# Optimization experiments

Hardware: AMD Instinct MI355X
Metric: run time of the kernel (lower is better)

Reference implementation:

```python
import jax, jax.numpy as jnp
import numpy as np

N, E, F_IN, DIM, HEADS = 16384, 262144, 128, 64, 4
HID = DIM * HEADS  # 256
NEG = 0.2


def _lin(k, fan_in, fan_out):
    kw, kb = jax.random.split(k)
    s = 1.0 / np.sqrt(fan_in)
    return (jax.random.uniform(kw, (fan_in, fan_out), jnp.float32, -s, s),
            jax.random.uniform(kb, (fan_out,), jnp.float32, -s, s))


def setup_inputs() -> dict:
    key = jax.random.key(0)
    ks = jax.random.split(key, 20)
    x = jax.random.normal(ks[0], (N, F_IN), jnp.float32)
    edge_index = jax.random.randint(ks[1], (2, E), 0, N, jnp.int32)
    Win, b_in = _lin(ks[2], F_IN, DIM)
    Wskip, bskip = _lin(ks[3], DIM, HID)
    # conv1: in=DIM, out per head=DIM, heads=HEADS, concat -> HID
    Wl1, _ = _lin(ks[4], DIM, HID)
    Wr1, _ = _lin(ks[5], DIM, HID)
    att1 = jax.random.normal(ks[6], (HEADS, DIM), jnp.float32) * 0.1
    b1 = jnp.zeros((HID,), jnp.float32)
    # conv2: in=HID, out=HID, heads=1, concat=False
    Wl2, _ = _lin(ks[7], HID, HID)
    Wr2, _ = _lin(ks[8], HID, HID)
    att2 = jax.random.normal(ks[9], (1, HID), jnp.float32) * 0.1
    b2 = jnp.zeros((HID,), jnp.float32)
    # conv3: in=HID, out=HID, heads=1, concat=False
    Wl3, _ = _lin(ks[10], HID, HID)
    Wr3, _ = _lin(ks[11], HID, HID)
    att3 = jax.random.normal(ks[12], (1, HID), jnp.float32) * 0.1
    b3 = jnp.zeros((HID,), jnp.float32)
    Wm1, bm1 = _lin(ks[13], HID, DIM)
    Wm2, bm2 = _lin(ks[14], DIM, DIM)
    Wm3, bm3 = _lin(ks[15], DIM, 1)
    return dict(x=x, edge_index=edge_index, Win=Win, b_in=b_in,
                Wskip=Wskip, bskip=bskip,
                Wl1=Wl1, Wr1=Wr1, att1=att1, b1=b1,
                Wl2=Wl2, Wr2=Wr2, att2=att2, b2=b2,
                Wl3=Wl3, Wr3=Wr3, att3=att3, b3=b3,
                Wm1=Wm1, bm1=bm1, Wm2=Wm2, bm2=bm2, Wm3=Wm3, bm3=bm3)


def gatv2(x, src, dst, Wl, Wr, att, b, concat):
    # PyG GATv2Conv: x_l = lin_l(x)[src], x_r = lin_r(x)[dst]
    n = x.shape[0]
    H, D = att.shape
    xl = (x @ Wl).reshape(n, H, D)
    xr = (x @ Wr).reshape(n, H, D)
    e = jax.nn.leaky_relu(xl[src] + xr[dst], NEG)          # [E, H, D]
    logits = jnp.einsum('ehd,hd->eh', e, att)              # [E, H]
    m = jax.ops.segment_max(logits, dst, num_segments=n)   # per-dst softmax
    alpha = jnp.exp(logits - m[dst])
    denom = jax.ops.segment_sum(alpha, dst, num_segments=n)
    alpha = alpha / denom[dst]
    out = jax.ops.segment_sum(alpha[:, :, None] * xl[src], dst, num_segments=n)
    out = out.reshape(n, H * D) if concat else out.mean(axis=1)
    return out + b


def reference(x, edge_index, Win, b_in, Wskip, bskip,
              Wl1, Wr1, att1, b1, Wl2, Wr2, att2, b2,
              Wl3, Wr3, att3, b3, Wm1, bm1, Wm2, bm2, Wm3, bm3):
    n = x.shape[0]
    # add self loops (GATv2Conv default add_self_loops=True)
    loop = jnp.arange(n, dtype=edge_index.dtype)
    src = jnp.concatenate([edge_index[0], loop])
    dst = jnp.concatenate([edge_index[1], loop])

    h = jax.nn.relu(x @ Win + b_in)                         # [N, DIM]
    out1 = jax.nn.relu(gatv2(h, src, dst, Wl1, Wr1, att1, b1, True))
    out1 = out1 + (h @ Wskip + bskip)                       # [N, HID]
    out2 = jax.nn.relu(gatv2(out1, src, dst, Wl2, Wr2, att2, b2, False))
    out2 = out2 + out1
    out3 = jax.nn.relu(gatv2(out2, src, dst, Wl3, Wr3, att3, b3, False))
    out3 = out3 + out2
    out = jax.nn.relu(out3 @ Wm1 + bm1)
    out = jax.nn.relu(out @ Wm2 + bm2)
    out = out @ Wm3 + bm3                                   # [N, 1]
    return out.reshape(-1)
```

## Files before the change

kernel.cpp:

```cpp
#include <hip/hip_runtime.h>
#include <cstdint>
#include <cstddef>

#define N_NODES 16384
#define E_EDGES 262144
#define FIN     128
#define DIM     64
#define HID     256
#define NEG     0.2f

typedef _Float16 h8 __attribute__((ext_vector_type(8)));
typedef _Float16 h4 __attribute__((ext_vector_type(4)));
typedef float    f32x4 __attribute__((ext_vector_type(4)));

__global__ __launch_bounds__(256) void zero_cnt_kernel(int4* __restrict__ cnt) {
    cnt[blockIdx.x * 256 + threadIdx.x] = make_int4(0, 0, 0, 0);
}

__global__ __launch_bounds__(256) void hist_kernel(const int* __restrict__ dst,
                                                   int* __restrict__ cnt) {
    int i = blockIdx.x * 256 + threadIdx.x;
    if (i < E_EDGES) atomicAdd(&cnt[dst[i]], 1);
}

__global__ __launch_bounds__(256) void csr_scan_kernel(const int* __restrict__ cnt,
                                                       int* __restrict__ offs,
                                                       int* __restrict__ cursor) {
    __shared__ int bs[256];
    __shared__ int psum[257];
    int tid = threadIdx.x;
    int base = tid * 64;
    int s = 0;
    for (int i = 0; i < 64; ++i) s += cnt[base + i];
    bs[tid] = s;
    __syncthreads();
    if (tid == 0) {
        int r = 0;
        for (int i = 0; i < 256; ++i) { psum[i] = r; r += bs[i]; }
        psum[256] = r;
    }
    __syncthreads();
    int run = psum[tid];
    for (int i = 0; i < 64; ++i) {
        int c = cnt[base + i];
        offs[base + i] = run;
        cursor[base + i] = run;
        run += c;
    }
    if (tid == 255) offs[N_NODES] = run;
}

__global__ __launch_bounds__(256) void scatter_kernel(const int* __restrict__ src,
                                                      const int* __restrict__ dst,
                                                      int* __restrict__ cursor,
                                                      int* __restrict__ esrc) {
    int i = blockIdx.x * 256 + threadIdx.x;
    if (i < E_EDGES) {
        int p = atomicAdd(&cursor[dst[i]], 1);
        esrc[p] = src[i];
    }
}

struct PackJob { const float* W; _Float16* dst; int Ksrc, Nsrc, NT, colOff; };
struct PackJobs { PackJob j[10]; };

__global__ __launch_bounds__(256) void pack_all_kernel(PackJobs jobs) {
    PackJob jb = jobs.j[blockIdx.y];
    int i = blockIdx.x * 256 + threadIdx.x;
    if (i < jb.Ksrc * jb.Nsrc) {
        int k = i / jb.Nsrc, n = i % jb.Nsrc;
        jb.dst[((size_t)(k >> 3) * jb.NT + jb.colOff + n) * 8 + (k & 7)] = (_Float16)jb.W[i];
    }
}

template<int K, bool RELU, bool O16, bool IN32>
__global__ __launch_bounds__(64) void mfma_n64_kernel(const void* __restrict__ Av,
                                                      const _Float16* __restrict__ Wp,
                                                      const float* __restrict__ bias,
                                                      void* __restrict__ outv) {
    int lane = threadIdx.x;
    int rowBase = blockIdx.x * 64;
    int l15 = lane & 15, l4 = lane >> 4;

    f32x4 acc[4][4] = {};
#pragma unroll
    for (int ks = 0; ks < K / 32; ++ks) {
        h8 af[4], bf[4];
#pragma unroll
        for (int mi = 0; mi < 4; ++mi) {
            if constexpr (IN32) {
                const float* ap = (const float*)Av + (size_t)(rowBase + mi * 16 + l15) * K + ks * 32 + l4 * 8;
                float4 a0 = *(const float4*)ap;
                float4 a1 = *(const float4*)(ap + 4);
                h8 v;
                v[0] = (_Float16)a0.x; v[1] = (_Float16)a0.y;
                v[2] = (_Float16)a0.z; v[3] = (_Float16)a0.w;
                v[4] = (_Float16)a1.x; v[5] = (_Float16)a1.y;
                v[6] = (_Float16)a1.z; v[7] = (_Float16)a1.w;
                af[mi] = v;
            } else {
                af[mi] = *(const h8*)((const _Float16*)Av + (size_t)(rowBase + mi * 16 + l15) * K + ks * 32 + l4 * 8);
            }
        }
#pragma unroll
        for (int ni = 0; ni < 4; ++ni)
            bf[ni] = *(const h8*)(Wp + ((size_t)(ks * 4 + l4) * 64 + ni * 16 + l15) * 8);
#pragma unroll
        for (int mi = 0; mi < 4; ++mi)
#pragma unroll
            for (int ni = 0; ni < 4; ++ni)
                acc[mi][ni] = __builtin_amdgcn_mfma_f32_16x16x32_f16(af[mi], bf[ni], acc[mi][ni], 0, 0, 0);
    }
#pragma unroll
    for (int mi = 0; mi < 4; ++mi)
#pragma unroll
        for (int ni = 0; ni < 4; ++ni) {
            int c = ni * 16 + l15;
            float bv = bias[c];
#pragma unroll
            for (int q = 0; q < 4; ++q) {
                int r = rowBase + mi * 16 + l4 * 4 + q;
                float v = acc[mi][ni][q] + bv;
                if (RELU) v = fmaxf(v, 0.f);
                if constexpr (O16) ((_Float16*)outv)[(size_t)r * 64 + c] = (_Float16)v;
                else               ((float*)outv)[(size_t)r * 64 + c] = v;
            }
        }
}

template<int K>
__global__ __launch_bounds__(256) void mfma_gemm_kernel(const _Float16* __restrict__ A,
                                                        const _Float16* __restrict__ Wp,
                                                        int NT,
                                                        _Float16* __restrict__ o16a,
                                                        _Float16* __restrict__ o16b,
                                                        float* __restrict__ o32,
                                                        const float* __restrict__ bias) {
    int tid = threadIdx.x;
    int lane = tid & 63, wid = tid >> 6;
    int wm = wid >> 1, wn = wid & 1;
    int rowBase = blockIdx.x * 128 + wm * 64;
    int colBase = blockIdx.y * 128 + wn * 64;
    int l15 = lane & 15, l4 = lane >> 4;

    f32x4 acc[4][4] = {};
#pragma unroll
    for (int ks = 0; ks < K / 32; ++ks) {
        h8 af[4], bf[4];
#pragma unroll
        for (int mi = 0; mi < 4; ++mi)
            af[mi] = *(const h8*)(A + (size_t)(rowBase + mi * 16 + l15) * K + ks * 32 + l4 * 8);
#pragma unroll
        for (int ni = 0; ni < 4; ++ni)
            bf[ni] = *(const h8*)(Wp + ((size_t)(ks * 4 + l4) * NT + colBase + ni * 16 + l15) * 8);
#pragma unroll
        for (int mi = 0; mi < 4; ++mi)
#pragma unroll
            for (int ni = 0; ni < 4; ++ni)
                acc[mi][ni] = __builtin_amdgcn_mfma_f32_16x16x32_f16(af[mi], bf[ni], acc[mi][ni], 0, 0, 0);
    }

    int seg = colBase >> 8;
    int cbase = colBase & 255;
    if (o32 != nullptr && seg == 2) {
#pragma unroll
        for (int mi = 0; mi < 4; ++mi)
#pragma unroll
            for (int ni = 0; ni < 4; ++ni) {
                int c = cbase + ni * 16 + l15;
                float bv = bias[c];
#pragma unroll
                for (int q = 0; q < 4; ++q) {
                    int r = rowBase + mi * 16 + l4 * 4 + q;
                    o32[(size_t)r * 256 + c] = acc[mi][ni][q] + bv;
                }
            }
    } else {
        _Float16* o = (seg == 0) ? o16a : o16b;
#pragma unroll
        for (int mi = 0; mi < 4; ++mi)
#pragma unroll
            for (int ni = 0; ni < 4; ++ni) {
                int c = cbase + ni * 16 + l15;
#pragma unroll
                for (int q = 0; q < 4; ++q) {
                    int r = rowBase + mi * 16 + l4 * 4 + q;
                    o[(size_t)r * 256 + c] = (_Float16)acc[mi][ni][q];
                }
            }
    }
}

template<int H, int OMODE>
__global__ __launch_bounds__(256) void gat_agg_kernel(const _Float16* __restrict__ xl,
                                                      const _Float16* __restrict__ xr,
                                                      const float* __restrict__ att,
                                                      const float* __restrict__ bias,
                                                      const float* __restrict__ resid,
                                                      const int* __restrict__ offs,
                                                      const int* __restrict__ esrc,
                                                      float* __restrict__ out,
                                                      _Float16* __restrict__ out16) {
    int wid = threadIdx.x >> 6;
    int lane = threadIdx.x & 63;
    int node = blockIdx.x * 4 + wid;

    auto ld4 = [&](const _Float16* p, int n) -> float4 {
        h4 v = *(const h4*)(p + ((size_t)n << 8) + (lane << 2));
        return make_float4((float)v[0], (float)v[1], (float)v[2], (float)v[3]);
    };

    float4 xrv = ld4(xr, node);
    float4 av = ((const float4*)att)[lane];

    float m = -1e30f, s = 0.f;
    float4 acc = make_float4(0.f, 0.f, 0.f, 0.f);

    auto logit = [&](const float4& xlv) -> float {
        float ex = xlv.x + xrv.x; ex = ex > 0.f ? ex : NEG * ex;
        float ey = xlv.y + xrv.y; ey = ey > 0.f ? ey : NEG * ey;
        float ez = xlv.z + xrv.z; ez = ez > 0.f ? ez : NEG * ez;
        float ew = xlv.w + xrv.w; ew = ew > 0.f ? ew : NEG * ew;
        float lp = ex * av.x + ey * av.y + ez * av.z + ew * av.w;
        lp += __shfl_xor(lp, 1);
        lp += __shfl_xor(lp, 2);
        lp += __shfl_xor(lp, 4);
        lp += __shfl_xor(lp, 8);
        if constexpr (H == 1) {
            lp += __shfl_xor(lp, 16);
            lp += __shfl_xor(lp, 32);
        }
        return lp;
    };

    auto single = [&](int src) {
        float4 xlv = ld4(xl, src);
        float lp = logit(xlv);
        float mn = fmaxf(m, lp);
        float c = __expf(m - mn);
        float p = __expf(lp - mn);
        s = s * c + p;
        acc.x = acc.x * c + p * xlv.x;
        acc.y = acc.y * c + p * xlv.y;
        acc.z = acc.z * c + p * xlv.z;
        acc.w = acc.w * c + p * xlv.w;
        m = mn;
    };

    single(node);
    int e0 = offs[node], e1 = offs[node + 1];
    int e = e0;
    for (; e + 8 <= e1; e += 8) {
        float4 xv[8]; float lp[8], pp[8];
#pragma unroll
        for (int j = 0; j < 8; ++j) xv[j] = ld4(xl, esrc[e + j]);
#pragma unroll
        for (int j = 0; j < 8; ++j) lp[j] = logit(xv[j]);
        float mn = m;
#pragma unroll
        for (int j = 0; j < 8; ++j) mn = fmaxf(mn, lp[j]);
        float c = __expf(m - mn);
#pragma unroll
        for (int j = 0; j < 8; ++j) pp[j] = __expf(lp[j] - mn);
        float ps = 0.f;
        float4 pa = make_float4(0.f, 0.f, 0.f, 0.f);
#pragma unroll
        for (int j = 0; j < 8; ++j) {
            ps += pp[j];
            pa.x += pp[j] * xv[j].x;
            pa.y += pp[j] * xv[j].y;
            pa.z += pp[j] * xv[j].z;
            pa.w += pp[j] * xv[j].w;
        }
        s = s * c + ps;
        acc.x = acc.x * c + pa.x;
        acc.y = acc.y * c + pa.y;
        acc.z = acc.z * c + pa.z;
        acc.w = acc.w * c + pa.w;
        m = mn;
    }
    for (; e + 4 <= e1; e += 4) {
        float4 xv[4]; float lp[4], pp[4];
#pragma unroll
        for (int j = 0; j < 4; ++j) xv[j] = ld4(xl, esrc[e + j]);
#pragma unroll
        for (int j = 0; j < 4; ++j) lp[j] = logit(xv[j]);
        float mn = fmaxf(fmaxf(fmaxf(lp[0], lp[1]), fmaxf(lp[2], lp[3])), m);
        float c = __expf(m - mn);
#pragma unroll
        for (int j = 0; j < 4; ++j) pp[j] = __expf(lp[j] - mn);
        s = s * c + ((pp[0] + pp[1]) + (pp[2] + pp[3]));
        acc.x = acc.x * c + ((pp[0] * xv[0].x + pp[1] * xv[1].x) + (pp[2] * xv[2].x + pp[3] * xv[3].x));
        acc.y = acc.y * c + ((pp[0] * xv[0].y + pp[1] * xv[1].y) + (pp[2] * xv[2].y + pp[3] * xv[3].y));
        acc.z = acc.z * c + ((pp[0] * xv[0].z + pp[1] * xv[1].z) + (pp[2] * xv[2].z + pp[3] * xv[3].z));
        acc.w = acc.w * c + ((pp[0] * xv[0].w + pp[1] * xv[1].w) + (pp[2] * xv[2].w + pp[3] * xv[3].w));
        m = mn;
    }
    for (; e < e1; ++e) single(esrc[e]);

    float inv = 1.f / s;
    float4 bv = ((const float4*)bias)[lane];
    float4 rv = ((const float4*)resid)[((size_t)node << 6) + lane];
    float4 o;
    o.x = fmaxf(acc.x * inv + bv.x, 0.f) + rv.x;
    o.y = fmaxf(acc.y * inv + bv.y, 0.f) + rv.y;
    o.z = fmaxf(acc.z * inv + bv.z, 0.f) + rv.z;
    o.w = fmaxf(acc.w * inv + bv.w, 0.f) + rv.w;
    if constexpr (OMODE != 2)
        ((float4*)out)[((size_t)node << 6) + lane] = o;
    if constexpr (OMODE != 0) {
        h4 ov;
        ov[0] = (_Float16)o.x; ov[1] = (_Float16)o.y;
        ov[2] = (_Float16)o.z; ov[3] = (_Float16)o.w;
        *(h4*)(out16 + ((size_t)node << 8) + (lane << 2)) = ov;
    }
}

__global__ __launch_bounds__(64) void mlp_head_kernel(const _Float16* __restrict__ A,
                                                      const _Float16* __restrict__ Wm1p,
                                                      const float* __restrict__ bm1,
                                                      const _Float16* __restrict__ Wm2p,
                                                      const float* __restrict__ bm2,
                                                      const float* __restrict__ Wm3,
                                                      const float* __restrict__ bm3,
                                                      float* __restrict__ out) {
    __shared__ _Float16 t1s[64][72];
    int lane = threadIdx.x;
    int rowBase = blockIdx.x * 64;
    int l15 = lane & 15, l4 = lane >> 4;

    f32x4 acc[4][4] = {};
#pragma unroll
    for (int ks = 0; ks < 8; ++ks) {
        h8 af[4], bf[4];
#pragma unroll
        for (int mi = 0; mi < 4; ++mi)
            af[mi] = *(const h8*)(A + (size_t)(rowBase + mi * 16 + l15) * 256 + ks * 32 + l4 * 8);
#pragma unroll
        for (int ni = 0; ni < 4; ++ni)
            bf[ni] = *(const h8*)(Wm1p + ((size_t)(ks * 4 + l4) * 64 + ni * 16 + l15) * 8);
#pragma unroll
        for (int mi = 0; mi < 4; ++mi)
#pragma unroll
            for (int ni = 0; ni < 4; ++ni)
                acc[mi][ni] = __builtin_amdgcn_mfma_f32_16x16x32_f16(af[mi], bf[ni], acc[mi][ni], 0, 0, 0);
    }
#pragma unroll
    for (int mi = 0; mi < 4; ++mi)
#pragma unroll
        for (int ni = 0; ni < 4; ++ni) {
            int c = ni * 16 + l15;
            float bv = bm1[c];
#pragma unroll
            for (int q = 0; q < 4; ++q)
                t1s[mi * 16 + l4 * 4 + q][c] = (_Float16)fmaxf(acc[mi][ni][q] + bv, 0.f);
        }

    f32x4 acc2[4][4] = {};
#pragma unroll
    for (int ks = 0; ks < 2; ++ks) {
        h8 af[4], bf[4];
#pragma unroll
        for (int mi = 0; mi < 4; ++mi)
            af[mi] = *(const h8*)&t1s[mi * 16 + l15][ks * 32 + l4 * 8];
#pragma unroll
        for (int ni = 0; ni < 4; ++ni)
            bf[ni] = *(const h8*)(Wm2p + ((size_t)(ks * 4 + l4) * 64 + ni * 16 + l15) * 8);
#pragma unroll
        for (int mi = 0; mi < 4; ++mi)
#pragma unroll
            for (int ni = 0; ni < 4; ++ni)
                acc2[mi][ni] = __builtin_amdgcn_mfma_f32_16x16x32_f16(af[mi], bf[ni], acc2[mi][ni], 0, 0, 0);
    }

    float b3 = bm3[0];
    float b2v[4], w3v[4];
#pragma unroll
    for (int ni = 0; ni < 4; ++ni) {
        b2v[ni] = bm2[ni * 16 + l15];
        w3v[ni] = Wm3[ni * 16 + l15];
    }
#pragma unroll
    for (int mi = 0; mi < 4; ++mi)
#pragma unroll
        for (int q = 0; q < 4; ++q) {
            float part = 0.f;
#pragma unroll
            for (int ni = 0; ni < 4; ++ni)
                part += fmaxf(acc2[mi][ni][q] + b2v[ni], 0.f) * w3v[ni];
            part += __shfl_xor(part, 1);
            part += __shfl_xor(part, 2);
            part += __shfl_xor(part, 4);
            part += __shfl_xor(part, 8);
            if (l15 == 0)
                out[rowBase + mi * 16 + l4 * 4 + q] = part + b3;
        }
}

extern "C" void kernel_launch(void* const* d_in, const int* in_sizes, int n_in,
                              void* d_out, int out_size, void* d_ws, size_t ws_size,
                              hipStream_t stream) {
    const float* x     = (const float*)d_in[0];
    const int*   ei    = (const int*)d_in[1];
    const float* Win   = (const float*)d_in[2];
    const float* b_in  = (const float*)d_in[3];
    const float* Wskip = (const float*)d_in[4];
    const float* bskip = (const float*)d_in[5];
    const float* Wl1   = (const float*)d_in[6];
    const float* Wr1   = (const float*)d_in[7];
    const float* att1  = (const float*)d_in[8];
    const float* b1    = (const float*)d_in[9];
    const float* Wl2   = (const float*)d_in[10];
    const float* Wr2   = (const float*)d_in[11];
    const float* att2  = (const float*)d_in[12];
    const float* b2    = (const float*)d_in[13];
    const float* Wl3   = (const float*)d_in[14];
    const float* Wr3   = (const float*)d_in[15];
    const float* att3  = (const float*)d_in[16];
    const float* b3    = (const float*)d_in[17];
    const float* Wm1   = (const float*)d_in[18];
    const float* bm1   = (const float*)d_in[19];
    const float* Wm2   = (const float*)d_in[20];
    const float* bm2   = (const float*)d_in[21];
    const float* Wm3   = (const float*)d_in[22];
    const float* bm3   = (const float*)d_in[23];

    char* p = (char*)d_ws;
    auto alloc = [&](size_t bytes) { char* r = p; p += (bytes + 255) & ~(size_t)255; return r; };
    const size_t NN = N_NODES;
    float*    skip = (float*)alloc(NN * 256 * 4);
    float*    out1 = (float*)alloc(NN * 256 * 4);
    _Float16* o116 = (_Float16*)alloc(NN * 256 * 2);
    _Float16* o216 = (_Float16*)alloc(NN * 256 * 2);
    _Float16* o316 = o116;
    _Float16* h16  = (_Float16*)alloc(NN * 64 * 2);
    _Float16* xl16 = (_Float16*)alloc(NN * 256 * 2);
    _Float16* xr16 = (_Float16*)alloc(NN * 256 * 2);
    _Float16* Wp1  = (_Float16*)alloc((size_t)64 * 768 * 2);
    _Float16* Wp2  = (_Float16*)alloc((size_t)256 * 512 * 2);
    _Float16* Wp3  = (_Float16*)alloc((size_t)256 * 512 * 2);
    _Float16* Winp = (_Float16*)alloc((size_t)128 * 64 * 2);
    _Float16* Wm1p = (_Float16*)alloc((size_t)256 * 64 * 2);
    _Float16* Wm2p = (_Float16*)alloc((size_t)64 * 64 * 2);
    int* cnt    = (int*)alloc(N_NODES * 4);
    int* offs   = (int*)alloc((N_NODES + 1) * 4);
    int* cursor = (int*)alloc(N_NODES * 4);
    int* esrc   = (int*)alloc(E_EDGES * 4);

    const int* src = ei;
    const int* dst = ei + E_EDGES;

    zero_cnt_kernel<<<N_NODES / 1024, 256, 0, stream>>>((int4*)cnt);
    hist_kernel<<<E_EDGES / 256, 256, 0, stream>>>(dst, cnt);
    csr_scan_kernel<<<1, 256, 0, stream>>>(cnt, offs, cursor);
    scatter_kernel<<<E_EDGES / 256, 256, 0, stream>>>(src, dst, cursor, esrc);

    PackJobs jobs = {{
        { Wl1,   Wp1,  64,  256, 768, 0   },
        { Wr1,   Wp1,  64,  256, 768, 256 },
        { Wskip, Wp1,  64,  256, 768, 512 },
        { Wl2,   Wp2,  256, 256, 512, 0   },
        { Wr2,   Wp2,  256, 256, 512, 256 },
        { Wl3,   Wp3,  256, 256, 512, 0   },
        { Wr3,   Wp3,  256, 256, 512, 256 },
        { Win,   Winp, 128, 64,  64,  0   },
        { Wm1,   Wm1p, 256, 64,  64,  0   },
        { Wm2,   Wm2p, 64,  64,  64,  0   },
    }};
    pack_all_kernel<<<dim3(256, 10), 256, 0, stream>>>(jobs);

    mfma_n64_kernel<128, true, true, true><<<N_NODES / 64, 64, 0, stream>>>(x, Winp, b_in, h16);

    mfma_gemm_kernel<64><<<dim3(128, 6), 256, 0, stream>>>(h16, Wp1, 768, xl16, xr16, skip, bskip);
    gat_agg_kernel<4, 1><<<N_NODES / 4, 256, 0, stream>>>(xl16, xr16, att1, b1, skip, offs, esrc, out1, o116);

    mfma_gemm_kernel<256><<<dim3(128, 4), 256, 0, stream>>>(o116, Wp2, 512, xl16, xr16, nullptr, nullptr);
    gat_agg_kernel<1, 1><<<N_NODES / 4, 256, 0, stream>>>(xl16, xr16, att2, b2, out1, offs, esrc, skip , o216);

    mfma_gemm_kernel<256><<<dim3(128, 4), 256, 0, stream>>>(o216, Wp3, 512, xl16, xr16, nullptr, nullptr);
    gat_agg_kernel<1, 2><<<N_NODES / 4, 256, 0, stream>>>(xl16, xr16, att3, b3, skip , offs, esrc, nullptr, o316);

    mlp_head_kernel<<<N_NODES / 64, 64, 0, stream>>>(o316, Wm1p, bm1, Wm2p, bm2, Wm3, bm3, (float*)d_out);
}
```

Baseline: 225.5 us.

## Split each node's edge aggregation across four waves with LDS softmax merge

The GAT aggregation kernel now assigns one block per destination node instead of one wave per node. The four waves take interleaved edges, keep their own online-softmax state, and merge it through shared memory using max rescaling. The goal is more parallelism per node and better load balance across uneven degrees, at the cost of a block barrier, LDS traffic, and three waves sitting idle during the final merge. The grid grows to N blocks.

```diff
diff --git a/kernel.cpp b/kernel.cpp
--- a/kernel.cpp
+++ b/kernel.cpp
@@ -201,9 +201,13 @@
                                                       const int* __restrict__ esrc,
                                                       float* __restrict__ out,
                                                       _Float16* __restrict__ out16) {
+    __shared__ float  lm[3][64];
+    __shared__ float  lssum[3][64];
+    __shared__ float4 lacc[3][64];
+
     int wid = threadIdx.x >> 6;
     int lane = threadIdx.x & 63;
-    int node = blockIdx.x * 4 + wid;
+    int node = blockIdx.x;
 
     auto ld4 = [&](const _Float16* p, int n) -> float4 {
         h4 v = *(const h4*)(p + ((size_t)n << 8) + (lane << 2));
@@ -247,42 +251,13 @@
         m = mn;
     };
 
-    single(node);
+    if (wid == 0) single(node);
     int e0 = offs[node], e1 = offs[node + 1];
-    int e = e0;
-    for (; e + 8 <= e1; e += 8) {
-        float4 xv[8]; float lp[8], pp[8];
-#pragma unroll
-        for (int j = 0; j < 8; ++j) xv[j] = ld4(xl, esrc[e + j]);
-#pragma unroll
-        for (int j = 0; j < 8; ++j) lp[j] = logit(xv[j]);
-        float mn = m;
-#pragma unroll
-        for (int j = 0; j < 8; ++j) mn = fmaxf(mn, lp[j]);
-        float c = __expf(m - mn);
-#pragma unroll
-        for (int j = 0; j < 8; ++j) pp[j] = __expf(lp[j] - mn);
-        float ps = 0.f;
-        float4 pa = make_float4(0.f, 0.f, 0.f, 0.f);
-#pragma unroll
-        for (int j = 0; j < 8; ++j) {
-            ps += pp[j];
-            pa.x += pp[j] * xv[j].x;
-            pa.y += pp[j] * xv[j].y;
-            pa.z += pp[j] * xv[j].z;
-            pa.w += pp[j] * xv[j].w;
-        }
-        s = s * c + ps;
-        acc.x = acc.x * c + pa.x;
-        acc.y = acc.y * c + pa.y;
-        acc.z = acc.z * c + pa.z;
-        acc.w = acc.w * c + pa.w;
-        m = mn;
-    }
-    for (; e + 4 <= e1; e += 4) {
+    int e = e0 + wid;
+    for (; e + 12 < e1; e += 16) {
         float4 xv[4]; float lp[4], pp[4];
 #pragma unroll
-        for (int j = 0; j < 4; ++j) xv[j] = ld4(xl, esrc[e + j]);
+        for (int j = 0; j < 4; ++j) xv[j] = ld4(xl, esrc[e + 4 * j]);
 #pragma unroll
         for (int j = 0; j < 4; ++j) lp[j] = logit(xv[j]);
         float mn = fmaxf(fmaxf(fmaxf(lp[0], lp[1]), fmaxf(lp[2], lp[3])), m);
@@ -296,16 +271,41 @@
         acc.w = acc.w * c + ((pp[0] * xv[0].w + pp[1] * xv[1].w) + (pp[2] * xv[2].w + pp[3] * xv[3].w));
         m = mn;
     }
-    for (; e < e1; ++e) single(esrc[e]);
-
-    float inv = 1.f / s;
+    for (; e < e1; e += 4) single(esrc[e]);
+
+    if (wid != 0) {
+        lm[wid - 1][lane] = m;
+        lssum[wid - 1][lane] = s;
+        lacc[wid - 1][lane] = acc;
+    }
+    __syncthreads();
+    if (wid != 0) return;
+
+    float M = m;
+#pragma unroll
+    for (int w = 0; w < 3; ++w) M = fmaxf(M, lm[w][lane]);
+    float c0 = __expf(m - M);
+    float stot = s * c0;
+    float4 atot = make_float4(acc.x * c0, acc.y * c0, acc.z * c0, acc.w * c0);
+#pragma unroll
+    for (int w = 0; w < 3; ++w) {
+        float cw = __expf(lm[w][lane] - M);
+        float4 aw = lacc[w][lane];
+        stot += lssum[w][lane] * cw;
+        atot.x += aw.x * cw;
+        atot.y += aw.y * cw;
+        atot.z += aw.z * cw;
+        atot.w += aw.w * cw;
+    }
+
+    float inv = 1.f / stot;
     float4 bv = ((const float4*)bias)[lane];
     float4 rv = ((const float4*)resid)[((size_t)node << 6) + lane];
     float4 o;
-    o.x = fmaxf(acc.x * inv + bv.x, 0.f) + rv.x;
-    o.y = fmaxf(acc.y * inv + bv.y, 0.f) + rv.y;
-    o.z = fmaxf(acc.z * inv + bv.z, 0.f) + rv.z;
-    o.w = fmaxf(acc.w * inv + bv.w, 0.f) + rv.w;
+    o.x = fmaxf(atot.x * inv + bv.x, 0.f) + rv.x;
+    o.y = fmaxf(atot.y * inv + bv.y, 0.f) + rv.y;
+    o.z = fmaxf(atot.z * inv + bv.z, 0.f) + rv.z;
+    o.w = fmaxf(atot.w * inv + bv.w, 0.f) + rv.w;
     if constexpr (OMODE != 2)
         ((float4*)out)[((size_t)node << 6) + lane] = o;
     if constexpr (OMODE != 0) {
@@ -472,13 +472,13 @@
     mfma_n64_kernel<128, true, true, true><<<N_NODES / 64, 64, 0, stream>>>(x, Winp, b_in, h16);
 
     mfma_gemm_kernel<64><<<dim3(128, 6), 256, 0, stream>>>(h16, Wp1, 768, xl16, xr16, skip, bskip);
-    gat_agg_kernel<4, 1><<<N_NODES / 4, 256, 0, stream>>>(xl16, xr16, att1, b1, skip, offs, esrc, out1, o116);
+    gat_agg_kernel<4, 1><<<N_NODES, 256, 0, stream>>>(xl16, xr16, att1, b1, skip, offs, esrc, out1, o116);
 
     mfma_gemm_kernel<256><<<dim3(128, 4), 256, 0, stream>>>(o116, Wp2, 512, xl16, xr16, nullptr, nullptr);
-    gat_agg_kernel<1, 1><<<N_NODES / 4, 256, 0, stream>>>(xl16, xr16, att2, b2, out1, offs, esrc, skip , o216);
+    gat_agg_kernel<1, 1><<<N_NODES, 256, 0, stream>>>(xl16, xr16, att2, b2, out1, offs, esrc, skip , o216);
 
     mfma_gemm_kernel<256><<<dim3(128, 4), 256, 0, stream>>>(o216, Wp3, 512, xl16, xr16, nullptr, nullptr);
-    gat_agg_kernel<1, 2><<<N_NODES / 4, 256, 0, stream>>>(xl16, xr16, att3, b3, skip , offs, esrc, nullptr, o316);
+    gat_agg_kernel<1, 2><<<N_NODES, 256, 0, stream>>>(xl16, xr16, att3, b3, skip , offs, esrc, nullptr, o316);
 
     mlp_head_kernel<<<N_NODES / 64, 64, 0, stream>>>(o316, Wm1p, bm1, Wm2p, bm2, Wm3, bm3, (float*)d_out);
 }
```

Measured after the change: 235.7 us. 1.05x slower.

## Split GAT aggregation wave into four edge groups with packed fp16 logits

Applied to the files above, without the earlier changes.

The GAT aggregation kernel now splits each wave into four 16-lane groups. Each group processes a different incoming edge, and each lane covers 16 feature dims loaded as two 16-byte vectors. The logit is computed in packed fp16 (add, leaky-relu via max, fdot2) with fewer shuffle steps per edge. Per-group online-softmax states are merged by an xor butterfly before the output is written. This cuts the serial per-edge dependency chain and the reduction cost, but drops the 8-edge batched ILP, adds a 16-value cross-group merge, and computes logits at reduced fp16 precision.

```diff
diff --git a/kernel.cpp b/kernel.cpp
--- a/kernel.cpp
+++ b/kernel.cpp
@@ -11,6 +11,7 @@
 
 typedef _Float16 h8 __attribute__((ext_vector_type(8)));
 typedef _Float16 h4 __attribute__((ext_vector_type(4)));
+typedef _Float16 h2 __attribute__((ext_vector_type(2)));
 typedef float    f32x4 __attribute__((ext_vector_type(4)));
 
 __global__ __launch_bounds__(256) void zero_cnt_kernel(int4* __restrict__ cnt) {
@@ -201,118 +202,110 @@
                                                       const int* __restrict__ esrc,
                                                       float* __restrict__ out,
                                                       _Float16* __restrict__ out16) {
-    int wid = threadIdx.x >> 6;
-    int lane = threadIdx.x & 63;
+    int tid = threadIdx.x;
+    int wid = tid >> 6;
+    int lane = tid & 63;
     int node = blockIdx.x * 4 + wid;
-
-    auto ld4 = [&](const _Float16* p, int n) -> float4 {
-        h4 v = *(const h4*)(p + ((size_t)n << 8) + (lane << 2));
-        return make_float4((float)v[0], (float)v[1], (float)v[2], (float)v[3]);
-    };
-
-    float4 xrv = ld4(xr, node);
-    float4 av = ((const float4*)att)[lane];
+    int g  = lane >> 4;
+    int li = lane & 15;
+
+    h2 xrv[8];
+    {
+        const h8* xp = (const h8*)(xr + ((size_t)node << 8) + (li << 4));
+        h8 a0 = xp[0], a1 = xp[1];
+#pragma unroll
+        for (int i = 0; i < 4; ++i) { xrv[i][0] = a0[2 * i]; xrv[i][1] = a0[2 * i + 1]; }
+#pragma unroll
+        for (int i = 0; i < 4; ++i) { xrv[4 + i][0] = a1[2 * i]; xrv[4 + i][1] = a1[2 * i + 1]; }
+    }
+    h2 attv[8];
+    {
+        const float4* ap = (const float4*)(att + (li << 4));
+#pragma unroll
+        for (int i = 0; i < 4; ++i) {
+            float4 a = ap[i];
+            attv[2 * i][0] = (_Float16)a.x; attv[2 * i][1] = (_Float16)a.y;
+            attv[2 * i + 1][0] = (_Float16)a.z; attv[2 * i + 1][1] = (_Float16)a.w;
+        }
+    }
+    const h2 negc = { (_Float16)NEG, (_Float16)NEG };
 
     float m = -1e30f, s = 0.f;
-    float4 acc = make_float4(0.f, 0.f, 0.f, 0.f);
-
-    auto logit = [&](const float4& xlv) -> float {
-        float ex = xlv.x + xrv.x; ex = ex > 0.f ? ex : NEG * ex;
-        float ey = xlv.y + xrv.y; ey = ey > 0.f ? ey : NEG * ey;
-        float ez = xlv.z + xrv.z; ez = ez > 0.f ? ez : NEG * ez;
-        float ew = xlv.w + xrv.w; ew = ew > 0.f ? ew : NEG * ew;
-        float lp = ex * av.x + ey * av.y + ez * av.z + ew * av.w;
-        lp += __shfl_xor(lp, 1);
-        lp += __shfl_xor(lp, 2);
-        lp += __shfl_xor(lp, 4);
-        lp += __shfl_xor(lp, 8);
+    float acc[16];
+#pragma unroll
+    for (int i = 0; i < 16; ++i) acc[i] = 0.f;
+
+    int e0 = offs[node];
+    int total = offs[node + 1] - e0 + 1;
+
+    for (int vi = g; vi < total; vi += 4) {
+        int srcn = (vi == 0) ? node : esrc[e0 + vi - 1];
+        const h8* xp = (const h8*)(xl + ((size_t)srcn << 8) + (li << 4));
+        h8 a0 = xp[0], a1 = xp[1];
+
+        float part = 0.f;
+        float xf[16];
+#pragma unroll
+        for (int i = 0; i < 8; ++i) {
+            h2 v;
+            if (i < 4) { v[0] = a0[2 * i]; v[1] = a0[2 * i + 1]; }
+            else       { v[0] = a1[2 * (i - 4)]; v[1] = a1[2 * (i - 4) + 1]; }
+            xf[2 * i]     = (float)v[0];
+            xf[2 * i + 1] = (float)v[1];
+            h2 sum = v + xrv[i];
+            h2 lr = __builtin_elementwise_max(sum, sum * negc);
+            part = __builtin_amdgcn_fdot2(lr, attv[i], part, false);
+        }
+        part += __shfl_xor(part, 1);
+        part += __shfl_xor(part, 2);
         if constexpr (H == 1) {
-            lp += __shfl_xor(lp, 16);
-            lp += __shfl_xor(lp, 32);
-        }
-        return lp;
-    };
-
-    auto single = [&](int src) {
-        float4 xlv = ld4(xl, src);
-        float lp = logit(xlv);
+            part += __shfl_xor(part, 4);
+            part += __shfl_xor(part, 8);
+        }
+        float lp = part;
+
         float mn = fmaxf(m, lp);
         float c = __expf(m - mn);
         float p = __expf(lp - mn);
         s = s * c + p;
-        acc.x = acc.x * c + p * xlv.x;
-        acc.y = acc.y * c + p * xlv.y;
-        acc.z = acc.z * c + p * xlv.z;
-        acc.w = acc.w * c + p * xlv.w;
+#pragma unroll
+        for (int i = 0; i < 16; ++i) acc[i] = acc[i] * c + p * xf[i];
         m = mn;
-    };
-
-    single(node);
-    int e0 = offs[node], e1 = offs[node + 1];
-    int e = e0;
-    for (; e + 8 <= e1; e += 8) {
-        float4 xv[8]; float lp[8], pp[8];
-#pragma unroll
-        for (int j = 0; j < 8; ++j) xv[j] = ld4(xl, esrc[e + j]);
-#pragma unroll
-        for (int j = 0; j < 8; ++j) lp[j] = logit(xv[j]);
-        float mn = m;
-#pragma unroll
-        for (int j = 0; j < 8; ++j) mn = fmaxf(mn, lp[j]);
-        float c = __expf(m - mn);
-#pragma unroll
-        for (int j = 0; j < 8; ++j) pp[j] = __expf(lp[j] - mn);
-        float ps = 0.f;
-        float4 pa = make_float4(0.f, 0.f, 0.f, 0.f);
-#pragma unroll
-        for (int j = 0; j < 8; ++j) {
-            ps += pp[j];
-            pa.x += pp[j] * xv[j].x;
-            pa.y += pp[j] * xv[j].y;
-            pa.z += pp[j] * xv[j].z;
-            pa.w += pp[j] * xv[j].w;
-        }
-        s = s * c + ps;
-        acc.x = acc.x * c + pa.x;
-        acc.y = acc.y * c + pa.y;
-        acc.z = acc.z * c + pa.z;
-        acc.w = acc.w * c + pa.w;
-        m = mn;
-    }
-    for (; e + 4 <= e1; e += 4) {
-        float4 xv[4]; float lp[4], pp[4];
-#pragma unroll
-        for (int j = 0; j < 4; ++j) xv[j] = ld4(xl, esrc[e + j]);
-#pragma unroll
-        for (int j = 0; j < 4; ++j) lp[j] = logit(xv[j]);
-        float mn = fmaxf(fmaxf(fmaxf(lp[0], lp[1]), fmaxf(lp[2], lp[3])), m);
-        float c = __expf(m - mn);
-#pragma unroll
-        for (int j = 0; j < 4; ++j) pp[j] = __expf(lp[j] - mn);
-        s = s * c + ((pp[0] + pp[1]) + (pp[2] + pp[3]));
-        acc.x = acc.x * c + ((pp[0] * xv[0].x + pp[1] * xv[1].x) + (pp[2] * xv[2].x + pp[3] * xv[3].x));
-        acc.y = acc.y * c + ((pp[0] * xv[0].y + pp[1] * xv[1].y) + (pp[2] * xv[2].y + pp[3] * xv[3].y));
-        acc.z = acc.z * c + ((pp[0] * xv[0].z + pp[1] * xv[1].z) + (pp[2] * xv[2].z + pp[3] * xv[3].z));
-        acc.w = acc.w * c + ((pp[0] * xv[0].w + pp[1] * xv[1].w) + (pp[2] * xv[2].w + pp[3] * xv[3].w));
-        m = mn;
-    }
-    for (; e < e1; ++e) single(esrc[e]);
+    }
+
+#pragma unroll
+    for (int mask = 16; mask <= 32; mask <<= 1) {
+        float m2 = __shfl_xor(m, mask);
+        float s2 = __shfl_xor(s, mask);
+        float M = fmaxf(m, m2);
+        float c1 = __expf(m - M);
+        float c2 = __expf(m2 - M);
+        s = s * c1 + s2 * c2;
+#pragma unroll
+        for (int i = 0; i < 16; ++i) {
+            float a2 = __shfl_xor(acc[i], mask);
+            acc[i] = acc[i] * c1 + a2 * c2;
+        }
+        m = M;
+    }
 
     float inv = 1.f / s;
-    float4 bv = ((const float4*)bias)[lane];
-    float4 rv = ((const float4*)resid)[((size_t)node << 6) + lane];
-    float4 o;
-    o.x = fmaxf(acc.x * inv + bv.x, 0.f) + rv.x;
-    o.y = fmaxf(acc.y * inv + bv.y, 0.f) + rv.y;
-    o.z = fmaxf(acc.z * inv + bv.z, 0.f) + rv.z;
-    o.w = fmaxf(acc.w * inv + bv.w, 0.f) + rv.w;
-    if constexpr (OMODE != 2)
-        ((float4*)out)[((size_t)node << 6) + lane] = o;
+    int dbase = (li << 4) + (g << 2);
+    float4 bv = *(const float4*)(bias + dbase);
+    float4 rv = *(const float4*)(resid + ((size_t)node << 8) + dbase);
+    float o0 = fmaxf(acc[(g << 2) + 0] * inv + bv.x, 0.f) + rv.x;
+    float o1 = fmaxf(acc[(g << 2) + 1] * inv + bv.y, 0.f) + rv.y;
+    float o2 = fmaxf(acc[(g << 2) + 2] * inv + bv.z, 0.f) + rv.z;
+    float o3 = fmaxf(acc[(g << 2) + 3] * inv + bv.w, 0.f) + rv.w;
+    if constexpr (OMODE != 2) {
+        float4 ov = make_float4(o0, o1, o2, o3);
+        *(float4*)(out + ((size_t)node << 8) + dbase) = ov;
+    }
     if constexpr (OMODE != 0) {
-        h4 ov;
-        ov[0] = (_Float16)o.x; ov[1] = (_Float16)o.y;
-        ov[2] = (_Float16)o.z; ov[3] = (_Float16)o.w;
-        *(h4*)(out16 + ((size_t)node << 8) + (lane << 2)) = ov;
+        h4 hv;
+        hv[0] = (_Float16)o0; hv[1] = (_Float16)o1;
+        hv[2] = (_Float16)o2; hv[3] = (_Float16)o3;
+        *(h4*)(out16 + ((size_t)node << 8) + dbase) = hv;
     }
 }
 
```

Result: faster. 209.1 us (-7.3%).
